# Optimization experiments

Hardware: AMD Instinct MI355X
Metric: run time of the kernel (lower is better)

## Reference

```python
import jax, jax.numpy as jnp
import numpy as np

B, P, D = 32, 64, 34
L = 1048576  # 1024x1024 flattened locations


def setup_inputs() -> dict:
    key = jax.random.key(0)
    k1, k2, k3, k4 = jax.random.split(key, 4)
    preds = jax.random.normal(k1, (B, L), dtype=jnp.float32)
    vals = jax.random.normal(k2, (B, P, D), dtype=jnp.float32)
    idx = jax.random.randint(k3, (B, P, D), 0, L).astype(jnp.float32)
    # valid flag > 0 with prob ~0.7; guarantee each image has at least one valid entry
    flags = jax.random.uniform(k4, (B, P, D), dtype=jnp.float32) - 0.3
    flags = flags.at[:, 0, 0].set(1.0)
    gts = jnp.stack([vals, idx, flags], axis=-1)  # [B, P, D, 3]
    return {"preds": preds, "gts": gts}


def reference(preds, gts):
    # gts[..., 0] = target value, gts[..., 1] = flat index into preds, gts[..., 2] = valid flag
    vals = gts[..., 0]                      # [B, P, D]
    idx = gts[..., 1].astype(jnp.int32)     # [B, P, D]
    valid = gts[..., 2] > 0                 # [B, P, D]
    b = preds.shape[0]
    gathered = jnp.take_along_axis(preds, idx.reshape(b, -1), axis=1).reshape(idx.shape)
    per = jnp.where(valid, jnp.abs(gathered - vals), jnp.zeros((), preds.dtype))
    # num_people = persons with at least one valid dim (others are skipped in the loop)
    num_people = jnp.sum(jnp.any(valid, axis=-1), axis=-1).astype(preds.dtype)  # [B]
    return jnp.sum(per, axis=(1, 2)) / num_people  # [B]
```

## Files before the change

### kernel.cpp

```cpp
#include <hip/hip_runtime.h>


#define B_ 32
#define P_ 64
#define D_ 34
#define L_ 1048576
#define GPB 4
#define BLK_PER_IMG (P_ / GPB)

__global__ __launch_bounds__(256) void reg_l1_main(
    const float* __restrict__ preds,
    const float* __restrict__ gts,
    float* __restrict__ ws) {
  const int g    = blockIdx.x;
  const int b    = blockIdx.y;
  const int wave = threadIdx.x >> 6;
  const int lane = threadIdx.x & 63;
  const int p    = g * GPB + wave;

  float contrib = 0.0f;
  int valid = 0;
  if (lane < D_) {
    const float* gt = gts + (((size_t)b * P_ + p) * D_ + lane) * 3;
    const float v    = gt[0];
    const float fidx = gt[1];
    const float flag = gt[2];
    if (flag > 0.0f) {
      const int idx = (int)fidx;
      contrib = fabsf(preds[(size_t)b * L_ + idx] - v);
      valid = 1;
    }
  }

  for (int off = 1; off < 64; off <<= 1) contrib += __shfl_xor(contrib, off);
  const unsigned long long bal = __ballot(valid);
  const float pcnt = (bal != 0ull) ? 1.0f : 0.0f;

  __shared__ float s_sum[GPB];
  __shared__ float s_cnt[GPB];
  if (lane == 0) {
    s_sum[wave] = contrib;
    s_cnt[wave] = pcnt;
  }
  __syncthreads();
  if (threadIdx.x == 0) {
    const float ts = s_sum[0] + s_sum[1] + s_sum[2] + s_sum[3];
    const float tc = s_cnt[0] + s_cnt[1] + s_cnt[2] + s_cnt[3];
    ws[b * BLK_PER_IMG + g] = ts;
    ws[B_ * BLK_PER_IMG + b * BLK_PER_IMG + g] = tc;
  }
}

__global__ __launch_bounds__(64) void reg_l1_final(
    const float* __restrict__ ws,
    float* __restrict__ out) {
  const int b    = blockIdx.x;
  const int lane = threadIdx.x;
  float s = 0.0f, c = 0.0f;
  if (lane < BLK_PER_IMG) {
    s = ws[b * BLK_PER_IMG + lane];
    c = ws[B_ * BLK_PER_IMG + b * BLK_PER_IMG + lane];
  }
  for (int off = 1; off < BLK_PER_IMG; off <<= 1) {
    s += __shfl_xor(s, off);
    c += __shfl_xor(c, off);
  }
  if (lane == 0) out[b] = s / c;
}

extern "C" void kernel_launch(void* const* d_in, const int* in_sizes, int n_in,
                              void* d_out, int out_size, void* d_ws, size_t ws_size,
                              hipStream_t stream) {
  const float* preds = (const float*)d_in[0];
  const float* gts   = (const float*)d_in[1];
  float* out = (float*)d_out;
  float* ws  = (float*)d_ws;

  dim3 grid(BLK_PER_IMG, B_);
  reg_l1_main<<<grid, 256, 0, stream>>>(preds, gts, ws);
  reg_l1_final<<<B_, 64, 0, stream>>>(ws, out);
}
```

Baseline: 164.1 us.

## Fuse final reduction into main kernel via atomics and last-block finish

Replaces the two-kernel scheme with a single pass. Each block atomically adds its partial sum and person count into per-image accumulators, and a completion counter lets the last block compute the final division. A memset clears the accumulators before launch. This removes the second kernel launch but adds atomics, a memset operation, and nondeterministic float summation order.

```diff
diff --git a/kernel.cpp b/kernel.cpp
--- a/kernel.cpp
+++ b/kernel.cpp
@@ -7,11 +7,13 @@
 #define L_ 1048576
 #define GPB 4
 #define BLK_PER_IMG (P_ / GPB)
+#define NBLOCKS (B_ * BLK_PER_IMG)
 
-__global__ __launch_bounds__(256) void reg_l1_main(
+__global__ __launch_bounds__(256) void reg_l1_onepass(
     const float* __restrict__ preds,
     const float* __restrict__ gts,
-    float* __restrict__ ws) {
+    float* __restrict__ ws,
+    float* __restrict__ out) {
   const int g    = blockIdx.x;
   const int b    = blockIdx.y;
   const int wave = threadIdx.x >> 6;
@@ -26,8 +28,7 @@
     const float fidx = gt[1];
     const float flag = gt[2];
     if (flag > 0.0f) {
-      const int idx = (int)fidx;
-      contrib = fabsf(preds[(size_t)b * L_ + idx] - v);
+      contrib = fabsf(preds[(size_t)b * L_ + (int)fidx] - v);
       valid = 1;
     }
   }
@@ -38,34 +39,30 @@
 
   __shared__ float s_sum[GPB];
   __shared__ float s_cnt[GPB];
+  __shared__ int   s_last;
   if (lane == 0) {
     s_sum[wave] = contrib;
     s_cnt[wave] = pcnt;
   }
   __syncthreads();
+
   if (threadIdx.x == 0) {
     const float ts = s_sum[0] + s_sum[1] + s_sum[2] + s_sum[3];
     const float tc = s_cnt[0] + s_cnt[1] + s_cnt[2] + s_cnt[3];
-    ws[b * BLK_PER_IMG + g] = ts;
-    ws[B_ * BLK_PER_IMG + b * BLK_PER_IMG + g] = tc;
+    atomicAdd(&ws[b], ts);
+    atomicAdd(&ws[B_ + b], tc);
+    __threadfence();
+    const int old = atomicAdd((int*)&ws[2 * B_], 1);
+    s_last = (old == NBLOCKS - 1) ? 1 : 0;
   }
-}
+  __syncthreads();
 
-__global__ __launch_bounds__(64) void reg_l1_final(
-    const float* __restrict__ ws,
-    float* __restrict__ out) {
-  const int b    = blockIdx.x;
-  const int lane = threadIdx.x;
-  float s = 0.0f, c = 0.0f;
-  if (lane < BLK_PER_IMG) {
-    s = ws[b * BLK_PER_IMG + lane];
-    c = ws[B_ * BLK_PER_IMG + b * BLK_PER_IMG + lane];
+  if (s_last && threadIdx.x < B_) {
+    const int i = threadIdx.x;
+    const float s = __hip_atomic_load(&ws[i],      __ATOMIC_ACQUIRE, __HIP_MEMORY_SCOPE_AGENT);
+    const float c = __hip_atomic_load(&ws[B_ + i], __ATOMIC_ACQUIRE, __HIP_MEMORY_SCOPE_AGENT);
+    out[i] = s / c;
   }
-  for (int off = 1; off < BLK_PER_IMG; off <<= 1) {
-    s += __shfl_xor(s, off);
-    c += __shfl_xor(c, off);
-  }
-  if (lane == 0) out[b] = s / c;
 }
 
 extern "C" void kernel_launch(void* const* d_in, const int* in_sizes, int n_in,
@@ -76,7 +73,7 @@
   float* out = (float*)d_out;
   float* ws  = (float*)d_ws;
 
+  hipMemsetAsync(ws, 0, (2 * B_ + 1) * sizeof(float), stream);
   dim3 grid(BLK_PER_IMG, B_);
-  reg_l1_main<<<grid, 256, 0, stream>>>(preds, gts, ws);
-  reg_l1_final<<<B_, 64, 0, stream>>>(ws, out);
+  reg_l1_onepass<<<grid, 256, 0, stream>>>(preds, gts, ws, out);
 }
```

Measured after the change: 173.7 us. +5.8%, slower.
